# Kernel optimization log

Measured on AMD Instinct MI355X. Metric: run time of the kernel, lower is better.

Reference implementation:

```python
import jax, jax.numpy as jnp
import numpy as np

EPS = 1e-8


def _cos_distance(a, b):
    # a, b: [1, c, hw] ; centered cosine distance matrix [1, hw, hw2]
    a = a - a.mean(axis=2, keepdims=True)
    b = b - b.mean(axis=2, keepdims=True)
    a_norm = jnp.sqrt((a * a).sum(axis=1, keepdims=True) + EPS)
    b_norm = jnp.sqrt((b * b).sum(axis=1, keepdims=True) + EPS)
    a = a / (a_norm + EPS)
    b = b / (b_norm + EPS)
    return 1.0 - jnp.einsum('bci,bcj->bij', a, b)


def _cos_loss(a, b):
    # a, b: [1, c, hw]; mean of (1 - cosine similarity along channel dim)
    a_norm = jnp.sqrt((a * a).sum(axis=1, keepdims=True))
    b_norm = jnp.sqrt((b * b).sum(axis=1, keepdims=True))
    a_t = a / (a_norm + EPS)
    b_t = b / (b_norm + EPS)
    cossim = (a_t * b_t).sum(axis=1)
    return (1.0 - cossim).mean()


def setup_inputs() -> dict:
    key = jax.random.key(0)
    k1, k2 = jax.random.split(key)
    x_feats = jax.random.normal(k1, (1, 768, 128, 128), dtype=jnp.float32)
    s_feats = jax.random.normal(k2, (1, 768, 128, 128), dtype=jnp.float32)
    return {"x_feats": x_feats, "s_feats": s_feats}


def reference(x_feats, s_feats):
    n, c, h, w = x_feats.shape
    a_flat = x_feats.reshape(n, c, h * w)          # [1, c, hw]
    b_flat = s_feats.reshape(n, c, -1)             # [1, c, hw2]
    # cdist + argmin retrieval (feat_replace)
    d_mat = _cos_distance(a_flat, b_flat)          # [1, hw, hw2] (~1 GB)
    z_best = jnp.argmin(d_mat, axis=2)             # [1, hw]
    target = b_flat[:, :, z_best[0]]               # gather NN swap -> [1, c, hw]
    # cosine loss between x feats and NN-replaced target feats
    nn_loss = _cos_loss(a_flat, target)
    return nn_loss
```

## Files before the change

kernel.cpp:

```cpp
#include <hip/hip_runtime.h>
#include <hip/hip_bf16.h>
#include <stdint.h>

#define C_DIM 768
#define HW 16384
#define EPSF 1e-8f
#define GPQ 256

typedef __attribute__((ext_vector_type(4))) int i32x4;

__global__ __launch_bounds__(256) void k_means(const float* __restrict__ x,
                                               const float* __restrict__ s,
                                               float* __restrict__ meanA,
                                               float* __restrict__ meanB) {
  int ch = blockIdx.x;
  const float* src = (ch < C_DIM) ? (x + (size_t)ch * HW) : (s + (size_t)(ch - C_DIM) * HW);
  int t = threadIdx.x;
  float acc = 0.f;
  for (int i = t; i < HW; i += 256) acc += src[i];
  __shared__ float red[256];
  red[t] = acc;
  __syncthreads();
  for (int o = 128; o > 0; o >>= 1) {
    if (t < o) red[t] += red[t + o];
    __syncthreads();
  }
  if (t == 0) {
    float m = red[0] * (1.0f / HW);
    if (ch < C_DIM) meanA[ch] = m; else meanB[ch - C_DIM] = m;
  }
}

__global__ __launch_bounds__(256) void k_prepq(const float* __restrict__ x,
                                               const float* __restrict__ s,
                                               const float* __restrict__ meanA,
                                               const float* __restrict__ meanB,
                                               float* __restrict__ qsaG,
                                               float* __restrict__ effG,
                                               float* __restrict__ invbnG,
                                               float* __restrict__ rawNA,
                                               float* __restrict__ rawNB,
                                               float* __restrict__ uG,
                                               float* __restrict__ vG,
                                               signed char* __restrict__ qa,
                                               signed char* __restrict__ Bp) {
  __shared__ float lma[C_DIM], lmb[C_DIM];
  __shared__ float red[7 * 256];
  __shared__ float la[64 * 33], lb[64 * 33];
  __shared__ float lsa[64], lsb[64];
  int t = threadIdx.x;
  int j0 = blockIdx.x * 64;
  for (int c = t; c < C_DIM; c += 256) { lma[c] = meanA[c]; lmb[c] = meanB[c]; }
  __syncthreads();

  {
    int pl = t & 63, cl = t >> 6;
    int p = j0 + pl;
    float maxa = 0.f, ssaR = 0.f, maxb = 0.f, ssbC = 0.f, ssbR = 0.f, uacc = 0.f, vacc = 0.f;
    for (int c = cl; c < C_DIM; c += 4) {
      float av = x[(size_t)c * HW + p];
      float bv = s[(size_t)c * HW + p];
      float ac = av - lma[c];
      float bc = bv - lmb[c];
      maxa = fmaxf(maxa, fabsf(ac));
      maxb = fmaxf(maxb, fabsf(bc));
      ssaR += av * av;
      ssbC += bc * bc;
      ssbR += bv * bv;
      uacc += ac * lmb[c];
      vacc += bc * lma[c];
    }
    red[t] = maxa; red[256 + t] = ssaR; red[512 + t] = maxb;
    red[768 + t] = ssbC; red[1024 + t] = ssbR; red[1280 + t] = uacc; red[1536 + t] = vacc;
    __syncthreads();
    if (t < 64) {
      float ma = fmaxf(fmaxf(red[t], red[t + 64]), fmaxf(red[t + 128], red[t + 192]));
      float sa = red[256 + t] + red[256 + t + 64] + red[256 + t + 128] + red[256 + t + 192];
      float mb = fmaxf(fmaxf(red[512 + t], red[512 + t + 64]), fmaxf(red[512 + t + 128], red[512 + t + 192]));
      float sc = red[768 + t] + red[768 + t + 64] + red[768 + t + 128] + red[768 + t + 192];
      float sb = red[1024 + t] + red[1024 + t + 64] + red[1024 + t + 128] + red[1024 + t + 192];
      float uu = red[1280 + t] + red[1280 + t + 64] + red[1280 + t + 128] + red[1280 + t + 192];
      float vv = red[1536 + t] + red[1536 + t + 64] + red[1536 + t + 128] + red[1536 + t + 192];
      ma = fmaxf(ma, 1e-20f);
      mb = fmaxf(mb, 1e-20f);
      float ib = 1.0f / (sqrtf(sc + EPSF) + EPSF);
      lsa[t] = 127.0f / ma;
      lsb[t] = 127.0f / mb;
      qsaG[j0 + t] = 127.0f / ma;
      effG[j0 + t] = (mb * (1.0f / 127.0f)) * ib;
      invbnG[j0 + t] = ib;
      rawNA[j0 + t] = sqrtf(sa);
      rawNB[j0 + t] = sqrtf(sb);
      uG[j0 + t] = uu;
      vG[j0 + t] = vv;
    }
  }

  int wj = t >> 2;
  int wk = (t & 3) * 8;
  int p = j0 + wj;
  __syncthreads();
  float sa = lsa[wj];
  float sb = lsb[wj];
  int g = p >> 4;
  int laneB = p & 15;

  for (int c0 = 0; c0 < C_DIM; c0 += 32) {
    __syncthreads();
#pragma unroll
    for (int sIt = 0; sIt < 8; ++sIt) {
      int idx = t + sIt * 256;
      int r = idx >> 6, cc = idx & 63;
      la[cc * 33 + r] = x[(size_t)(c0 + r) * HW + j0 + cc];
      lb[cc * 33 + r] = s[(size_t)(c0 + r) * HW + j0 + cc];
    }
    __syncthreads();
    unsigned long long pkA = 0, pkB = 0;
#pragma unroll
    for (int uu = 0; uu < 8; ++uu) {
      int c = c0 + wk + uu;
      float av = (la[wj * 33 + wk + uu] - lma[c]) * sa;
      float bv = (lb[wj * 33 + wk + uu] - lmb[c]) * sb;
      int qA = (int)rintf(fminf(fmaxf(av, -127.f), 127.f));
      int qB = (int)rintf(fminf(fmaxf(bv, -127.f), 127.f));
      pkA |= ((unsigned long long)(unsigned char)(signed char)qA) << (8 * uu);
      pkB |= ((unsigned long long)(unsigned char)(signed char)qB) << (8 * uu);
    }
    *(unsigned long long*)(qa + (size_t)p * C_DIM + c0 + wk) = pkA;
    int k0 = c0 + wk;
    int sblk = k0 >> 6;
    int quad = (k0 & 63) >> 4;
    int e0 = k0 & 15;
    *(unsigned long long*)(Bp + (size_t)(g * 12 + sblk) * 1024 + (laneB | (quad << 4)) * 16 + e0) = pkB;
  }
}

__device__ __forceinline__ void gl_lds16(const void* g, void* l) {
  __builtin_amdgcn_global_load_lds((const __attribute__((address_space(1))) uint32_t*)g,
                                   (__attribute__((address_space(3))) uint32_t*)l, 16, 0, 0);
}

__global__ __launch_bounds__(256, 2) void k_gemm_argmax(
    const signed char* __restrict__ qa,
    const signed char* __restrict__ Bp,
    const float* __restrict__ eff,
    unsigned long long* __restrict__ best) {
  __shared__ signed char ringS[4 * 12288];
  __shared__ float effL[4096];
  int t = threadIdx.x;
  int lane = t & 63, w = t >> 6;
  int m = lane & 15, q = lane >> 4;
  int b = blockIdx.x;
  int xcd = b & 7;
  int bq = xcd >> 1;
  int rg = (b >> 3) | ((xcd & 1) << 6);
  int i0 = rg * 128;
  int g0 = bq * GPQ;
  int lane16 = lane * 16;
  int sW0 = (3 * w) * 1024 + lane16;

  const i32x4* qaV = (const i32x4*)qa;
  i32x4 a_res[2][12];
#pragma unroll
  for (int tm = 0; tm < 2; ++tm) {
    int row = i0 + w * 32 + tm * 16 + m;
#pragma unroll
    for (int s = 0; s < 12; ++s)
      a_res[tm][s] = qaV[(size_t)row * 48 + s * 4 + q];
  }

  {
    const signed char* ps = Bp + ((size_t)g0 * 12 + 3 * w) * 1024 + lane16;
#pragma unroll
    for (int gp = 0; gp < 3; ++gp) {
      signed char* dst = ringS + gp * 12288;
      gl_lds16(ps, dst + sW0);
      gl_lds16(ps + 1024, dst + sW0 + 1024);
      gl_lds16(ps + 2048, dst + sW0 + 2048);
      ps += 12288;
    }
  }
  for (int i = t; i < 4096; i += 256) effL[i] = eff[(g0 << 4) + i];
  __syncthreads();

  const signed char* srcW = Bp + ((size_t)(g0 + 3) * 12 + 3 * w) * 1024 + lane16;

  float bestv[2][4];
  int bestj[2][4];
#pragma unroll
  for (int tm = 0; tm < 2; ++tm)
#pragma unroll
    for (int r = 0; r < 4; ++r) { bestv[tm][r] = -3.0e38f; bestj[tm][r] = 0x7FFFFFFF; }

  int effOff = m;
  int jj = (g0 << 4) + m;

#define BODY(RB, VMSTR, DOSTAGE)                                                   \
  {                                                                                \
    asm volatile(VMSTR ::: "memory");                                              \
    __builtin_amdgcn_s_barrier();                                                  \
    const signed char* rb = ringS + (RB) * 12288;                                  \
    i32x4 f[12];                                                                   \
    _Pragma("unroll")                                                              \
    for (int s = 0; s < 12; ++s)                                                   \
      f[s] = *(const i32x4*)(rb + s * 1024 + lane16);                              \
    float ecur = effL[effOff];                                                     \
    i32x4 acc0 = {0, 0, 0, 0}, acc1 = {0, 0, 0, 0};                                \
    _Pragma("unroll")                                                              \
    for (int s = 0; s < 12; ++s) {                                                 \
      acc0 = __builtin_amdgcn_mfma_i32_16x16x64_i8(a_res[0][s], f[s], acc0, 0, 0, 0); \
      acc1 = __builtin_amdgcn_mfma_i32_16x16x64_i8(a_res[1][s], f[s], acc1, 0, 0, 0); \
    }                                                                              \
    if (DOSTAGE) {                                                                 \
      signed char* dst = ringS + (((RB) + 3) & 3) * 12288;                         \
      gl_lds16(srcW, dst + sW0);                                                   \
      gl_lds16(srcW + 1024, dst + sW0 + 1024);                                     \
      gl_lds16(srcW + 2048, dst + sW0 + 2048);                                     \
      srcW += 12288;                                                               \
    }                                                                              \
    _Pragma("unroll")                                                              \
    for (int r = 0; r < 4; ++r) {                                                  \
      float v0 = (float)acc0[r] * ecur;                                            \
      float v1 = (float)acc1[r] * ecur;                                            \
      if (v0 > bestv[0][r]) { bestv[0][r] = v0; bestj[0][r] = jj; }                \
      if (v1 > bestv[1][r]) { bestv[1][r] = v1; bestj[1][r] = jj; }                \
    }                                                                              \
    effOff += 16;                                                                  \
    jj += 16;                                                                      \
  }

  for (int mi = 0; mi < 63; ++mi) {
    BODY(0, "s_waitcnt vmcnt(6)", 1)
    BODY(1, "s_waitcnt vmcnt(6)", 1)
    BODY(2, "s_waitcnt vmcnt(6)", 1)
    BODY(3, "s_waitcnt vmcnt(6)", 1)
  }
  BODY(0, "s_waitcnt vmcnt(6)", 1)
  BODY(1, "s_waitcnt vmcnt(6)", 0)
  BODY(2, "s_waitcnt vmcnt(3)", 0)
  BODY(3, "s_waitcnt vmcnt(0)", 0)
#undef BODY

#pragma unroll
  for (int tm = 0; tm < 2; ++tm) {
#pragma unroll
    for (int r = 0; r < 4; ++r) {
      float bv = bestv[tm][r];
      int bj = bestj[tm][r];
#pragma unroll
      for (int off = 1; off < 16; off <<= 1) {
        float ov = __shfl_xor(bv, off, 64);
        int oj = __shfl_xor(bj, off, 64);
        if (ov > bv || (ov == bv && oj < bj)) { bv = ov; bj = oj; }
      }
      if (m == 0) {
        int i = i0 + w * 32 + tm * 16 + q * 4 + r;
        unsigned key = __float_as_uint(bv);
        key = (key & 0x80000000u) ? ~key : (key | 0x80000000u);
        unsigned long long packed =
            ((unsigned long long)key << 32) | (unsigned long long)(0xFFFFFFFFu - (unsigned)bj);
        atomicMax(&best[i], packed);
      }
    }
  }
}

__global__ __launch_bounds__(256) void k_loss2(const float* __restrict__ meanA,
                                               const float* __restrict__ meanB,
                                               const unsigned long long* __restrict__ best,
                                               const float* __restrict__ rawNA,
                                               const float* __restrict__ rawNB,
                                               const float* __restrict__ invbn,
                                               const float* __restrict__ qsa,
                                               const float* __restrict__ u,
                                               const float* __restrict__ v,
                                               float* __restrict__ out) {
  __shared__ float red[256];
  int t = threadIdx.x;
  float wp = 0.f;
  for (int c = t; c < C_DIM; c += 256) wp += meanA[c] * meanB[c];
  red[t] = wp;
  __syncthreads();
  for (int o = 128; o > 0; o >>= 1) {
    if (t < o) red[t] += red[t + o];
    __syncthreads();
  }
  float wdot = red[0];
  __syncthreads();

  int i = blockIdx.x * 256 + t;
  unsigned long long pk = best[i];
  unsigned key = (unsigned)(pk >> 32);
  unsigned fb = (key & 0x80000000u) ? (key & 0x7FFFFFFFu) : ~key;
  float bv = __uint_as_float(fb);
  int j = (int)(0xFFFFFFFFu - (unsigned)(pk & 0xFFFFFFFFull));
  float dotcc = bv / (invbn[j] * qsa[i]);
  float dot = dotcc + u[i] + v[j] + wdot;
  float cs = dot / ((rawNA[i] + EPSF) * (rawNB[j] + EPSF));
  red[t] = (1.0f - cs) * (1.0f / HW);
  __syncthreads();
  for (int o = 128; o > 0; o >>= 1) {
    if (t < o) red[t] += red[t + o];
    __syncthreads();
  }
  if (t == 0) atomicAdd(out, red[0]);
}

extern "C" void kernel_launch(void* const* d_in, const int* in_sizes, int n_in,
                              void* d_out, int out_size, void* d_ws, size_t ws_size,
                              hipStream_t stream) {
  const float* x = (const float*)d_in[0];
  const float* s = (const float*)d_in[1];
  char* ws = (char*)d_ws;
  float* meanA = (float*)(ws + 0);
  float* meanB = (float*)(ws + 4096);
  float* rawNA = (float*)(ws + 8192);
  float* rawNB = (float*)(ws + 73728);
  float* eff   = (float*)(ws + 139264);
  float* qsa   = (float*)(ws + 204800);
  float* invbn = (float*)(ws + 335872);
  float* u     = (float*)(ws + 401408);
  float* v     = (float*)(ws + 466944);
  unsigned long long* best = (unsigned long long*)(ws + 532480);
  signed char* qa = (signed char*)(ws + 663552);
  signed char* Bp = (signed char*)(ws + 663552 + 12582912);
  float* out = (float*)d_out;

  hipMemsetAsync(best, 0, HW * sizeof(unsigned long long), stream);
  hipMemsetAsync(out, 0, sizeof(float), stream);
  k_means<<<2 * C_DIM, 256, 0, stream>>>(x, s, meanA, meanB);
  k_prepq<<<HW / 64, 256, 0, stream>>>(x, s, meanA, meanB, qsa, eff, invbn, rawNA, rawNB, u, v, qa, Bp);
  k_gemm_argmax<<<512, 256, 0, stream>>>(qa, Bp, eff, best);
  k_loss2<<<HW / 256, 256, 0, stream>>>(meanA, meanB, best, rawNA, rawNB, invbn, qsa, u, v, out);
}
```

Baseline: 400.9 us.

## Software-pipeline LDS fragment loads in int8 GEMM and restage quantization via int8 LDS

```diff
diff --git a/kernel.cpp b/kernel.cpp
--- a/kernel.cpp
+++ b/kernel.cpp
@@ -15,9 +15,13 @@
                                                float* __restrict__ meanB) {
   int ch = blockIdx.x;
   const float* src = (ch < C_DIM) ? (x + (size_t)ch * HW) : (s + (size_t)(ch - C_DIM) * HW);
+  const float4* src4 = (const float4*)src;
   int t = threadIdx.x;
   float acc = 0.f;
-  for (int i = t; i < HW; i += 256) acc += src[i];
+  for (int i = t; i < HW / 4; i += 256) {
+    float4 v = src4[i];
+    acc += v.x + v.y + v.z + v.w;
+  }
   __shared__ float red[256];
   red[t] = acc;
   __syncthreads();
@@ -46,7 +50,8 @@
                                                signed char* __restrict__ Bp) {
   __shared__ float lma[C_DIM], lmb[C_DIM];
   __shared__ float red[7 * 256];
-  __shared__ float la[64 * 33], lb[64 * 33];
+  __shared__ signed char tA8[64 * 40];
+  __shared__ signed char tB8[64 * 40];
   __shared__ float lsa[64], lsb[64];
   int t = threadIdx.x;
   int j0 = blockIdx.x * 64;
@@ -95,43 +100,45 @@
       vG[j0 + t] = vv;
     }
   }
-
-  int wj = t >> 2;
-  int wk = (t & 3) * 8;
-  int p = j0 + wj;
-  __syncthreads();
-  float sa = lsa[wj];
-  float sb = lsb[wj];
-  int g = p >> 4;
-  int laneB = p & 15;
+  __syncthreads();
+
+  int cc = t & 63;
+  int r4 = t >> 6;
+  float sa = lsa[cc];
+  float sb = lsb[cc];
+  int pS = t >> 2;
+  int ch8 = (t & 3) * 8;
+  int pgS = j0 + pS;
+  int gS = pgS >> 4, laneS = pgS & 15;
 
   for (int c0 = 0; c0 < C_DIM; c0 += 32) {
     __syncthreads();
 #pragma unroll
-    for (int sIt = 0; sIt < 8; ++sIt) {
-      int idx = t + sIt * 256;
-      int r = idx >> 6, cc = idx & 63;
-      la[cc * 33 + r] = x[(size_t)(c0 + r) * HW + j0 + cc];
-      lb[cc * 33 + r] = s[(size_t)(c0 + r) * HW + j0 + cc];
-    }
-    __syncthreads();
-    unsigned long long pkA = 0, pkB = 0;
-#pragma unroll
-    for (int uu = 0; uu < 8; ++uu) {
-      int c = c0 + wk + uu;
-      float av = (la[wj * 33 + wk + uu] - lma[c]) * sa;
-      float bv = (lb[wj * 33 + wk + uu] - lmb[c]) * sb;
-      int qA = (int)rintf(fminf(fmaxf(av, -127.f), 127.f));
-      int qB = (int)rintf(fminf(fmaxf(bv, -127.f), 127.f));
-      pkA |= ((unsigned long long)(unsigned char)(signed char)qA) << (8 * uu);
-      pkB |= ((unsigned long long)(unsigned char)(signed char)qB) << (8 * uu);
-    }
-    *(unsigned long long*)(qa + (size_t)p * C_DIM + c0 + wk) = pkA;
-    int k0 = c0 + wk;
+    for (int v = 0; v < 2; ++v) {
+      int q4 = r4 + 4 * v;
+      unsigned pa = 0, pb = 0;
+#pragma unroll
+      for (int uu = 0; uu < 4; ++uu) {
+        int c = c0 + q4 * 4 + uu;
+        float av = (x[(size_t)c * HW + j0 + cc] - lma[c]) * sa;
+        float bv = (s[(size_t)c * HW + j0 + cc] - lmb[c]) * sb;
+        int qA = (int)rintf(fminf(fmaxf(av, -127.f), 127.f));
+        int qB = (int)rintf(fminf(fmaxf(bv, -127.f), 127.f));
+        pa |= ((unsigned)(unsigned char)(signed char)qA) << (8 * uu);
+        pb |= ((unsigned)(unsigned char)(signed char)qB) << (8 * uu);
+      }
+      *(unsigned*)&tA8[cc * 40 + q4 * 4] = pa;
+      *(unsigned*)&tB8[cc * 40 + q4 * 4] = pb;
+    }
+    __syncthreads();
+    unsigned long long va = *(const unsigned long long*)&tA8[pS * 40 + ch8];
+    *(unsigned long long*)(qa + (size_t)pgS * C_DIM + c0 + ch8) = va;
+    unsigned long long vb = *(const unsigned long long*)&tB8[pS * 40 + ch8];
+    int k0 = c0 + ch8;
     int sblk = k0 >> 6;
     int quad = (k0 & 63) >> 4;
     int e0 = k0 & 15;
-    *(unsigned long long*)(Bp + (size_t)(g * 12 + sblk) * 1024 + (laneB | (quad << 4)) * 16 + e0) = pkB;
+    *(unsigned long long*)(Bp + (size_t)(gS * 12 + sblk) * 1024 + (laneS | (quad << 4)) * 16 + e0) = vb;
   }
 }
 
@@ -195,29 +202,43 @@
   int effOff = m;
   int jj = (g0 << 4) + m;
 
-#define BODY(RB, VMSTR, DOSTAGE)                                                   \
+  i32x4 fA[6], fB[6];
+#pragma unroll
+  for (int s = 0; s < 6; ++s) fA[s] = *(const i32x4*)(ringS + s * 1024 + lane16);
+
+#define BODY(SLOT, VMSTR, DOSTAGE, DOAHEAD)                                        \
   {                                                                                \
     asm volatile(VMSTR ::: "memory");                                              \
     __builtin_amdgcn_s_barrier();                                                  \
-    const signed char* rb = ringS + (RB) * 12288;                                  \
-    i32x4 f[12];                                                                   \
+    const signed char* rb = ringS + (SLOT) * 12288;                                \
     _Pragma("unroll")                                                              \
-    for (int s = 0; s < 12; ++s)                                                   \
-      f[s] = *(const i32x4*)(rb + s * 1024 + lane16);                              \
-    float ecur = effL[effOff];                                                     \
-    i32x4 acc0 = {0, 0, 0, 0}, acc1 = {0, 0, 0, 0};                                \
-    _Pragma("unroll")                                                              \
-    for (int s = 0; s < 12; ++s) {                                                 \
-      acc0 = __builtin_amdgcn_mfma_i32_16x16x64_i8(a_res[0][s], f[s], acc0, 0, 0, 0); \
-      acc1 = __builtin_amdgcn_mfma_i32_16x16x64_i8(a_res[1][s], f[s], acc1, 0, 0, 0); \
-    }                                                                              \
+    for (int s = 0; s < 6; ++s)                                                    \
+      fB[s] = *(const i32x4*)(rb + (6 + s) * 1024 + lane16);                       \
     if (DOSTAGE) {                                                                 \
-      signed char* dst = ringS + (((RB) + 3) & 3) * 12288;                         \
+      signed char* dst = ringS + (((SLOT) + 3) & 3) * 12288;                       \
       gl_lds16(srcW, dst + sW0);                                                   \
       gl_lds16(srcW + 1024, dst + sW0 + 1024);                                     \
       gl_lds16(srcW + 2048, dst + sW0 + 2048);                                     \
       srcW += 12288;                                                               \
     }                                                                              \
+    i32x4 acc0 = {0, 0, 0, 0}, acc1 = {0, 0, 0, 0};                                \
+    _Pragma("unroll")                                                              \
+    for (int s = 0; s < 6; ++s) {                                                  \
+      acc0 = __builtin_amdgcn_mfma_i32_16x16x64_i8(a_res[0][s], fA[s], acc0, 0, 0, 0); \
+      acc1 = __builtin_amdgcn_mfma_i32_16x16x64_i8(a_res[1][s], fA[s], acc1, 0, 0, 0); \
+    }                                                                              \
+    if (DOAHEAD) {                                                                 \
+      const signed char* rn = ringS + (((SLOT) + 1) & 3) * 12288;                  \
+      _Pragma("unroll")                                                            \
+      for (int s = 0; s < 6; ++s)                                                  \
+        fA[s] = *(const i32x4*)(rn + s * 1024 + lane16);                           \
+    }                                                                              \
+    _Pragma("unroll")                                                              \
+    for (int s = 0; s < 6; ++s) {                                                  \
+      acc0 = __builtin_amdgcn_mfma_i32_16x16x64_i8(a_res[0][6 + s], fB[s], acc0, 0, 0, 0); \
+      acc1 = __builtin_amdgcn_mfma_i32_16x16x64_i8(a_res[1][6 + s], fB[s], acc1, 0, 0, 0); \
+    }                                                                              \
+    float ecur = effL[effOff];                                                     \
     _Pragma("unroll")                                                              \
     for (int r = 0; r < 4; ++r) {                                                  \
       float v0 = (float)acc0[r] * ecur;                                            \
@@ -230,15 +251,15 @@
   }
 
   for (int mi = 0; mi < 63; ++mi) {
-    BODY(0, "s_waitcnt vmcnt(6)", 1)
-    BODY(1, "s_waitcnt vmcnt(6)", 1)
-    BODY(2, "s_waitcnt vmcnt(6)", 1)
-    BODY(3, "s_waitcnt vmcnt(6)", 1)
-  }
-  BODY(0, "s_waitcnt vmcnt(6)", 1)
-  BODY(1, "s_waitcnt vmcnt(6)", 0)
-  BODY(2, "s_waitcnt vmcnt(3)", 0)
-  BODY(3, "s_waitcnt vmcnt(0)", 0)
+    BODY(0, "s_waitcnt vmcnt(3)", 1, 1)
+    BODY(1, "s_waitcnt vmcnt(3)", 1, 1)
+    BODY(2, "s_waitcnt vmcnt(3)", 1, 1)
+    BODY(3, "s_waitcnt vmcnt(3)", 1, 1)
+  }
+  BODY(0, "s_waitcnt vmcnt(3)", 1, 1)
+  BODY(1, "s_waitcnt vmcnt(3)", 0, 1)
+  BODY(2, "s_waitcnt vmcnt(0)", 0, 1)
+  BODY(3, "s_waitcnt vmcnt(0)", 0, 0)
 #undef BODY
 
 #pragma unroll
```

After: 393.3 us. About the same (-1.9%).

## Split prep kernel into stats and quantize kernels, vectorize mean loads

Applied to the files above, without the earlier changes.

```diff
diff --git a/kernel.cpp b/kernel.cpp
--- a/kernel.cpp
+++ b/kernel.cpp
@@ -15,9 +15,13 @@
                                                float* __restrict__ meanB) {
   int ch = blockIdx.x;
   const float* src = (ch < C_DIM) ? (x + (size_t)ch * HW) : (s + (size_t)(ch - C_DIM) * HW);
+  const float4* src4 = (const float4*)src;
   int t = threadIdx.x;
   float acc = 0.f;
-  for (int i = t; i < HW; i += 256) acc += src[i];
+  for (int i = t; i < HW / 4; i += 256) {
+    float4 v = src4[i];
+    acc += v.x + v.y + v.z + v.w;
+  }
   __shared__ float red[256];
   red[t] = acc;
   __syncthreads();
@@ -31,107 +35,122 @@
   }
 }
 
-__global__ __launch_bounds__(256) void k_prepq(const float* __restrict__ x,
+__global__ __launch_bounds__(256) void k_stats(const float* __restrict__ x,
                                                const float* __restrict__ s,
                                                const float* __restrict__ meanA,
                                                const float* __restrict__ meanB,
                                                float* __restrict__ qsaG,
+                                               float* __restrict__ qsbG,
                                                float* __restrict__ effG,
                                                float* __restrict__ invbnG,
                                                float* __restrict__ rawNA,
                                                float* __restrict__ rawNB,
                                                float* __restrict__ uG,
-                                               float* __restrict__ vG,
+                                               float* __restrict__ vG) {
+  __shared__ float lma[C_DIM], lmb[C_DIM];
+  __shared__ float red[7 * 256];
+  int t = threadIdx.x;
+  int p0 = blockIdx.x * 32;
+  for (int c = t; c < C_DIM; c += 256) { lma[c] = meanA[c]; lmb[c] = meanB[c]; }
+  __syncthreads();
+  int pl = t & 31, cl = t >> 5;
+  int p = p0 + pl;
+  float maxa = 0.f, ssaR = 0.f, maxb = 0.f, ssbC = 0.f, ssbR = 0.f, uacc = 0.f, vacc = 0.f;
+  for (int c = cl; c < C_DIM; c += 8) {
+    float av = x[(size_t)c * HW + p];
+    float bv = s[(size_t)c * HW + p];
+    float ac = av - lma[c];
+    float bc = bv - lmb[c];
+    maxa = fmaxf(maxa, fabsf(ac));
+    maxb = fmaxf(maxb, fabsf(bc));
+    ssaR += av * av;
+    ssbC += bc * bc;
+    ssbR += bv * bv;
+    uacc += ac * lmb[c];
+    vacc += bc * lma[c];
+  }
+  red[t] = maxa; red[256 + t] = ssaR; red[512 + t] = maxb;
+  red[768 + t] = ssbC; red[1024 + t] = ssbR; red[1280 + t] = uacc; red[1536 + t] = vacc;
+  __syncthreads();
+  if (t < 32) {
+    float ma = 0.f, sa = 0.f, mb = 0.f, sc = 0.f, sb = 0.f, uu = 0.f, vv = 0.f;
+#pragma unroll
+    for (int k = 0; k < 8; ++k) {
+      int idx = t + k * 32;
+      ma = fmaxf(ma, red[idx]);
+      sa += red[256 + idx];
+      mb = fmaxf(mb, red[512 + idx]);
+      sc += red[768 + idx];
+      sb += red[1024 + idx];
+      uu += red[1280 + idx];
+      vv += red[1536 + idx];
+    }
+    ma = fmaxf(ma, 1e-20f);
+    mb = fmaxf(mb, 1e-20f);
+    float ib = 1.0f / (sqrtf(sc + EPSF) + EPSF);
+    qsaG[p0 + t] = 127.0f / ma;
+    qsbG[p0 + t] = 127.0f / mb;
+    effG[p0 + t] = (mb * (1.0f / 127.0f)) * ib;
+    invbnG[p0 + t] = ib;
+    rawNA[p0 + t] = sqrtf(sa);
+    rawNB[p0 + t] = sqrtf(sb);
+    uG[p0 + t] = uu;
+    vG[p0 + t] = vv;
+  }
+}
+
+__global__ __launch_bounds__(256) void k_quant(const float* __restrict__ x,
+                                               const float* __restrict__ s,
+                                               const float* __restrict__ meanA,
+                                               const float* __restrict__ meanB,
+                                               const float* __restrict__ qsa,
+                                               const float* __restrict__ qsb,
                                                signed char* __restrict__ qa,
                                                signed char* __restrict__ Bp) {
   __shared__ float lma[C_DIM], lmb[C_DIM];
-  __shared__ float red[7 * 256];
-  __shared__ float la[64 * 33], lb[64 * 33];
-  __shared__ float lsa[64], lsb[64];
-  int t = threadIdx.x;
-  int j0 = blockIdx.x * 64;
+  __shared__ signed char tA8[32 * 72];
+  __shared__ signed char tB8[32 * 72];
+  int t = threadIdx.x;
+  int j0 = blockIdx.x * 32;
   for (int c = t; c < C_DIM; c += 256) { lma[c] = meanA[c]; lmb[c] = meanB[c]; }
-  __syncthreads();
-
-  {
-    int pl = t & 63, cl = t >> 6;
-    int p = j0 + pl;
-    float maxa = 0.f, ssaR = 0.f, maxb = 0.f, ssbC = 0.f, ssbR = 0.f, uacc = 0.f, vacc = 0.f;
-    for (int c = cl; c < C_DIM; c += 4) {
-      float av = x[(size_t)c * HW + p];
-      float bv = s[(size_t)c * HW + p];
-      float ac = av - lma[c];
-      float bc = bv - lmb[c];
-      maxa = fmaxf(maxa, fabsf(ac));
-      maxb = fmaxf(maxb, fabsf(bc));
-      ssaR += av * av;
-      ssbC += bc * bc;
-      ssbR += bv * bv;
-      uacc += ac * lmb[c];
-      vacc += bc * lma[c];
+
+  int cc = t & 31;
+  int r8 = t >> 5;
+  float sa = qsa[j0 + cc];
+  float sb = qsb[j0 + cc];
+  int pS = t >> 3;
+  int ch8 = (t & 7) * 8;
+  int pgS = j0 + pS;
+  int gS = pgS >> 4, laneS = pgS & 15;
+
+  for (int c0 = 0; c0 < C_DIM; c0 += 64) {
+    __syncthreads();
+#pragma unroll
+    for (int v = 0; v < 2; ++v) {
+      int q4 = r8 + 8 * v;
+      unsigned pa = 0, pb = 0;
+#pragma unroll
+      for (int uu = 0; uu < 4; ++uu) {
+        int c = c0 + q4 * 4 + uu;
+        float av = (x[(size_t)c * HW + j0 + cc] - lma[c]) * sa;
+        float bv = (s[(size_t)c * HW + j0 + cc] - lmb[c]) * sb;
+        int qA = (int)rintf(fminf(fmaxf(av, -127.f), 127.f));
+        int qB = (int)rintf(fminf(fmaxf(bv, -127.f), 127.f));
+        pa |= ((unsigned)(unsigned char)(signed char)qA) << (8 * uu);
+        pb |= ((unsigned)(unsigned char)(signed char)qB) << (8 * uu);
+      }
+      *(unsigned*)&tA8[cc * 72 + q4 * 4] = pa;
+      *(unsigned*)&tB8[cc * 72 + q4 * 4] = pb;
     }
-    red[t] = maxa; red[256 + t] = ssaR; red[512 + t] = maxb;
-    red[768 + t] = ssbC; red[1024 + t] = ssbR; red[1280 + t] = uacc; red[1536 + t] = vacc;
-    __syncthreads();
-    if (t < 64) {
-      float ma = fmaxf(fmaxf(red[t], red[t + 64]), fmaxf(red[t + 128], red[t + 192]));
-      float sa = red[256 + t] + red[256 + t + 64] + red[256 + t + 128] + red[256 + t + 192];
-      float mb = fmaxf(fmaxf(red[512 + t], red[512 + t + 64]), fmaxf(red[512 + t + 128], red[512 + t + 192]));
-      float sc = red[768 + t] + red[768 + t + 64] + red[768 + t + 128] + red[768 + t + 192];
-      float sb = red[1024 + t] + red[1024 + t + 64] + red[1024 + t + 128] + red[1024 + t + 192];
-      float uu = red[1280 + t] + red[1280 + t + 64] + red[1280 + t + 128] + red[1280 + t + 192];
-      float vv = red[1536 + t] + red[1536 + t + 64] + red[1536 + t + 128] + red[1536 + t + 192];
-      ma = fmaxf(ma, 1e-20f);
-      mb = fmaxf(mb, 1e-20f);
-      float ib = 1.0f / (sqrtf(sc + EPSF) + EPSF);
-      lsa[t] = 127.0f / ma;
-      lsb[t] = 127.0f / mb;
-      qsaG[j0 + t] = 127.0f / ma;
-      effG[j0 + t] = (mb * (1.0f / 127.0f)) * ib;
-      invbnG[j0 + t] = ib;
-      rawNA[j0 + t] = sqrtf(sa);
-      rawNB[j0 + t] = sqrtf(sb);
-      uG[j0 + t] = uu;
-      vG[j0 + t] = vv;
-    }
-  }
-
-  int wj = t >> 2;
-  int wk = (t & 3) * 8;
-  int p = j0 + wj;
-  __syncthreads();
-  float sa = lsa[wj];
-  float sb = lsb[wj];
-  int g = p >> 4;
-  int laneB = p & 15;
-
-  for (int c0 = 0; c0 < C_DIM; c0 += 32) {
-    __syncthreads();
-#pragma unroll
-    for (int sIt = 0; sIt < 8; ++sIt) {
-      int idx = t + sIt * 256;
-      int r = idx >> 6, cc = idx & 63;
-      la[cc * 33 + r] = x[(size_t)(c0 + r) * HW + j0 + cc];
-      lb[cc * 33 + r] = s[(size_t)(c0 + r) * HW + j0 + cc];
-    }
-    __syncthreads();
-    unsigned long long pkA = 0, pkB = 0;
-#pragma unroll
-    for (int uu = 0; uu < 8; ++uu) {
-      int c = c0 + wk + uu;
-      float av = (la[wj * 33 + wk + uu] - lma[c]) * sa;
-      float bv = (lb[wj * 33 + wk + uu] - lmb[c]) * sb;
-      int qA = (int)rintf(fminf(fmaxf(av, -127.f), 127.f));
-      int qB = (int)rintf(fminf(fmaxf(bv, -127.f), 127.f));
-      pkA |= ((unsigned long long)(unsigned char)(signed char)qA) << (8 * uu);
-      pkB |= ((unsigned long long)(unsigned char)(signed char)qB) << (8 * uu);
-    }
-    *(unsigned long long*)(qa + (size_t)p * C_DIM + c0 + wk) = pkA;
-    int k0 = c0 + wk;
+    __syncthreads();
+    unsigned long long va = *(const unsigned long long*)&tA8[pS * 72 + ch8];
+    *(unsigned long long*)(qa + (size_t)pgS * C_DIM + c0 + ch8) = va;
+    unsigned long long vb = *(const unsigned long long*)&tB8[pS * 72 + ch8];
+    int k0 = c0 + ch8;
     int sblk = k0 >> 6;
     int quad = (k0 & 63) >> 4;
     int e0 = k0 & 15;
-    *(unsigned long long*)(Bp + (size_t)(g * 12 + sblk) * 1024 + (laneB | (quad << 4)) * 16 + e0) = pkB;
+    *(unsigned long long*)(Bp + (size_t)(gS * 12 + sblk) * 1024 + (laneS | (quad << 4)) * 16 + e0) = vb;
   }
 }
 
@@ -318,6 +337,7 @@
   float* rawNB = (float*)(ws + 73728);
   float* eff   = (float*)(ws + 139264);
   float* qsa   = (float*)(ws + 204800);
+  float* qsb   = (float*)(ws + 270336);
   float* invbn = (float*)(ws + 335872);
   float* u     = (float*)(ws + 401408);
   float* v     = (float*)(ws + 466944);
@@ -329,7 +349,8 @@
   hipMemsetAsync(best, 0, HW * sizeof(unsigned long long), stream);
   hipMemsetAsync(out, 0, sizeof(float), stream);
   k_means<<<2 * C_DIM, 256, 0, stream>>>(x, s, meanA, meanB);
-  k_prepq<<<HW / 64, 256, 0, stream>>>(x, s, meanA, meanB, qsa, eff, invbn, rawNA, rawNB, u, v, qa, Bp);
+  k_stats<<<HW / 32, 256, 0, stream>>>(x, s, meanA, meanB, qsa, qsb, eff, invbn, rawNA, rawNB, u, v);
+  k_quant<<<HW / 32, 256, 0, stream>>>(x, s, meanA, meanB, qsa, qsb, qa, Bp);
   k_gemm_argmax<<<512, 256, 0, stream>>>(qa, Bp, eff, best);
   k_loss2<<<HW / 256, 256, 0, stream>>>(meanA, meanB, best, rawNA, rawNB, invbn, qsa, u, v, out);
 }
```

Result: faster. 356.3 us (-11.1%).
